# Kernel optimization log

Hardware: AMD Instinct MI355X
Metric: run time of the kernel (lower is better)

## Reference

```python
import jax, jax.numpy as jnp
import numpy as np

N_ACTOR = 128
NUM_MODS = 6
NUM_PTS = 30
N = 32768
B = 64
EPS = 1e-5


def _gn(x, g, b):
    # torch GroupNorm(1, C) on [..., C]: normalize over channel axis, affine
    m = jnp.mean(x, axis=-1, keepdims=True)
    v = jnp.mean((x - m) ** 2, axis=-1, keepdims=True)
    return (x - m) * jax.lax.rsqrt(v + EPS) * g + b


def setup_inputs() -> dict:
    key = jax.random.key(0)
    ks = jax.random.split(key, 32)
    d = N_ACTOR
    M = NUM_MODS
    s = 0.05
    rn = lambda k, shp: jax.random.normal(k, shp, jnp.float32) * s
    inp = {
        'actors': jax.random.normal(ks[0], (N, d), jnp.float32),
        'actor_ctrs': jax.random.normal(ks[1], (N, 2), jnp.float32),
        'actor_idcs': jnp.arange(N, dtype=jnp.int32).reshape(B, N // B),
        # per-mode residual MLP + output linear (stacked over modes)
        'pred_W1': rn(ks[2], (M, d, d)),
        'pred_g1': jnp.ones((M, d), jnp.float32),
        'pred_b1': jnp.zeros((M, d), jnp.float32),
        'pred_W2': rn(ks[3], (M, d, d)),
        'pred_g2': jnp.ones((M, d), jnp.float32),
        'pred_b2': jnp.zeros((M, d), jnp.float32),
        'pred_Wo': rn(ks[4], (M, d, 2 * NUM_PTS)),
        'pred_bo': rn(ks[5], (M, 2 * NUM_PTS)),
        # cls head: residual MLP + Linear(d,1)
        'cls_W1': rn(ks[6], (d, d)),
        'cls_g1': jnp.ones((d,), jnp.float32),
        'cls_b1': jnp.zeros((d,), jnp.float32),
        'cls_W2': rn(ks[7], (d, d)),
        'cls_g2': jnp.ones((d,), jnp.float32),
        'cls_b2': jnp.zeros((d,), jnp.float32),
        'cls_Wo': rn(ks[8], (d, 1)),
        'cls_bo': rn(ks[9], (1,)),
        # AttDest
        'att_dW1': rn(ks[10], (2, d)),
        'att_db1': rn(ks[11], (d,)),
        'att_dW2': rn(ks[12], (d, d)),
        'att_dg2': jnp.ones((d,), jnp.float32),
        'att_db2': jnp.zeros((d,), jnp.float32),
        'att_aW': rn(ks[13], (2 * d, d)),
        'att_ag': jnp.ones((d,), jnp.float32),
        'att_ab': jnp.zeros((d,), jnp.float32),
    }
    return inp


def reference(actors, actor_ctrs, actor_idcs, pred_W1, pred_g1, pred_b1,
              pred_W2, pred_g2, pred_b2, pred_Wo, pred_bo,
              cls_W1, cls_g1, cls_b1, cls_W2, cls_g2, cls_b2, cls_Wo, cls_bo,
              att_dW1, att_db1, att_dW2, att_dg2, att_db2,
              att_aW, att_ag, att_ab):
    n = actors.shape[0]
    M = pred_W1.shape[0]
    h = jnp.einsum('nc,mcd->mnd', actors, pred_W1)              # [M,N,d]
    h = jax.nn.relu(_gn(h, pred_g1[:, None, :], pred_b1[:, None, :]))
    h = _gn(jnp.einsum('mnd,mde->mne', h, pred_W2),
            pred_g2[:, None, :], pred_b2[:, None, :])
    h = jax.nn.relu(h + actors[None])                           # residual
    preds = jnp.einsum('mnd,mdo->mno', h, pred_Wo) + pred_bo[:, None, :]
    reg = preds.transpose(1, 0, 2).reshape(n, M, NUM_PTS, 2)    # [N,M,T,2]
    # per-scene reg[idcs] += ctrs: actor_idcs partitions arange(N), so this
    # is exactly a per-actor broadcast add of the (concatenated) centers
    reg = reg + actor_ctrs[:, None, None, :]
    dest_ctrs = jax.lax.stop_gradient(reg[:, :, -1, :])         # .detach()
    # --- AttDest ---
    dist = (actor_ctrs[:, None, :] - dest_ctrs).reshape(-1, 2)  # [N*M,2]
    dist = jax.nn.relu(dist @ att_dW1 + att_db1)
    dist = jax.nn.relu(_gn(dist @ att_dW2, att_dg2, att_db2))
    agts = jnp.broadcast_to(actors[:, None, :], (n, M, actors.shape[1]))
    agts = agts.reshape(-1, actors.shape[1])
    feats = jax.nn.relu(_gn(jnp.concatenate([dist, agts], axis=1) @ att_aW,
                            att_ag, att_ab))                    # [N*M,d]
    # --- cls head ---
    c = jax.nn.relu(_gn(feats @ cls_W1, cls_g1, cls_b1))
    c = _gn(c @ cls_W2, cls_g2, cls_b2)
    c = jax.nn.relu(c + feats)
    cls = (c @ cls_Wo + cls_bo).reshape(n, M)
    # --- sort modes by descending score, reorder reg accordingly ---
    order = jnp.argsort(-cls, axis=1)
    cls = jnp.take_along_axis(cls, order, axis=1)
    reg = jnp.take_along_axis(reg, order[:, :, None, None], axis=1)
    # train_model=True concatenates the per-scene splits back in order,
    # which reproduces the full arrays
    return cls, reg
```

## Files before the change

kernel.cpp:

```cpp
#include <hip/hip_runtime.h>

#define EPSV 1e-5f
#define CLS_SZ (32768*6)

#define AIDX(k,r) (((k)<<6) + ((r) ^ (((k)&15)<<2)))

__device__ __forceinline__ float4 ld4(const float* p) { return *reinterpret_cast<const float4*>(p); }
__device__ __forceinline__ void st4(float* p, float4 v) { *reinterpret_cast<float4*>(p) = v; }

__device__ __forceinline__ void fma48(float4 x, float4 wl, float4 wh, float acc[4][8]) {
  float av[4] = {x.x, x.y, x.z, x.w};
  float wv[8] = {wl.x, wl.y, wl.z, wl.w, wh.x, wh.y, wh.z, wh.w};
  #pragma unroll
  for (int r = 0; r < 4; ++r)
    #pragma unroll
    for (int c = 0; c < 8; ++c)
      acc[r][c] = fmaf(av[r], wv[c], acc[r][c]);
}

__device__ __forceinline__ void gemm128c(const float* __restrict__ X,
                                         const float* __restrict__ Wg,
                                         float* __restrict__ WB0, float* __restrict__ WB1,
                                         float acc[4][8], int ag4, int jg4, int tid)
{
  float4 rA = ld4(Wg + tid*4);
  float4 rB = ld4(Wg + 1024 + tid*4);
  __syncthreads();
  st4(WB0 + tid*4, rA);
  st4(WB1 + tid*4, rB);
  __syncthreads();
  #pragma unroll 1
  for (int c = 0; c < 16; ++c) {
    float4 rN;
    const bool pf = (c + 2 < 16);
    if (pf) rN = ld4(Wg + (c+2)*1024 + tid*4);
    const float* WB = (c & 1) ? WB1 : WB0;
    #pragma unroll
    for (int kk = 0; kk < 8; ++kk) {
      int k = c*8 + kk;
      float4 x  = ld4(X + ((k<<6) + (ag4 ^ ((k&15)<<2))));
      float4 wl = ld4(WB + (kk<<7) + jg4);
      float4 wh = ld4(WB + (kk<<7) + 64 + jg4);
      fma48(x, wl, wh, acc);
    }
    __syncthreads();
    if (pf) st4(((c & 1) ? WB1 : WB0) + tid*4, rN);
  }
}

__device__ __forceinline__ void gemm128wo(const float* __restrict__ X,
                                          const float* __restrict__ Wg,
                                          float* __restrict__ WB0, float* __restrict__ WB1,
                                          float acc[4][4], int ag4, int jg4, int tid)
{
  const bool act = tid < 120;
  const int row = tid / 15, col = (tid % 15) * 4;
  float4 rA, rB;
  if (act) { rA = ld4(Wg + row*60 + col); rB = ld4(Wg + 480 + row*60 + col); }
  __syncthreads();
  if (act) { st4(WB0 + (row<<6) + col, rA); st4(WB1 + (row<<6) + col, rB); }
  __syncthreads();
  #pragma unroll 1
  for (int c = 0; c < 16; ++c) {
    float4 rN;
    const bool pf = act && (c + 2 < 16);
    if (pf) rN = ld4(Wg + (c+2)*480 + row*60 + col);
    const float* WB = (c & 1) ? WB1 : WB0;
    #pragma unroll
    for (int kk = 0; kk < 8; ++kk) {
      int k = c*8 + kk;
      float4 x = ld4(X + ((k<<6) + (ag4 ^ ((k&15)<<2))));
      float4 w = ld4(WB + (kk<<6) + jg4);
      float av[4] = {x.x, x.y, x.z, x.w};
      float wv[4] = {w.x, w.y, w.z, w.w};
      #pragma unroll
      for (int r = 0; r < 4; ++r)
        #pragma unroll
        for (int cc = 0; cc < 4; ++cc)
          acc[r][cc] = fmaf(av[r], wv[cc], acc[r][cc]);
    }
    __syncthreads();
    if (pf) st4(((c & 1) ? WB1 : WB0) + (row<<6) + col, rN);
  }
}

__device__ __forceinline__ void gn_reduce(const float acc[4][8], float* PS1, float* PS2,
                                          float* MEAN, float* RSTD, int ag4, int jg, int tid)
{
  #pragma unroll
  for (int r = 0; r < 4; ++r) {
    float s = 0.f, q = 0.f;
    #pragma unroll
    for (int c = 0; c < 8; ++c) { float v = acc[r][c]; s += v; q += v*v; }
    s += __shfl_xor(s, 1, 64); q += __shfl_xor(q, 1, 64);
    s += __shfl_xor(s, 2, 64); q += __shfl_xor(q, 2, 64);
    PS1[(ag4+r)*5 + (jg>>2)] = s;
    PS2[(ag4+r)*5 + (jg>>2)] = q;
  }
  __syncthreads();
  if (tid < 64) {
    float a = 0.f, b = 0.f;
    #pragma unroll
    for (int j = 0; j < 4; ++j) { a += PS1[tid*5 + j]; b += PS2[tid*5 + j]; }
    float mu = a * 0.0078125f;
    float var = b * 0.0078125f - mu*mu;
    MEAN[tid] = mu;
    RSTD[tid] = rsqrtf(var + EPSV);
  }
  __syncthreads();
}

__global__ void __launch_bounds__(256) pred_kernel(
    const float* __restrict__ actors, const float* __restrict__ ctrs,
    const float* __restrict__ W1, const float* __restrict__ g1v, const float* __restrict__ b1v,
    const float* __restrict__ W2, const float* __restrict__ g2v, const float* __restrict__ b2v,
    const float* __restrict__ Wo, const float* __restrict__ bov,
    float* __restrict__ out_reg)
{
  __shared__ __align__(16) float ACTORS[8192];
  __shared__ __align__(16) float ACT[8192];
  __shared__ __align__(16) float WB0[1024], WB1[1024];
  __shared__ float PS1[320], PS2[320], MEAN[64], RSTD[64];

  const int tid = threadIdx.x;
  const int jg = tid & 15, ag = tid >> 4;
  const int jg4 = jg*4, ag4 = ag*4;
  const int m  = blockIdx.y;
  const int n0 = blockIdx.x * 64;

  #pragma unroll
  for (int p = 0; p < 8; ++p) {
    int i = (p<<8) + tid;
    int r = i >> 5, c4 = (i & 31) << 2;
    float4 v = ld4(actors + (size_t)(n0 + r)*128 + c4);
    ACTORS[((c4+0)<<6) + (r ^ ((((c4+0))&15)<<2))] = v.x;
    ACTORS[((c4+1)<<6) + (r ^ ((((c4+1))&15)<<2))] = v.y;
    ACTORS[((c4+2)<<6) + (r ^ ((((c4+2))&15)<<2))] = v.z;
    ACTORS[((c4+3)<<6) + (r ^ ((((c4+3))&15)<<2))] = v.w;
  }

  float acc[4][8];
  #pragma unroll
  for (int r = 0; r < 4; ++r)
    #pragma unroll
    for (int c = 0; c < 8; ++c) acc[r][c] = 0.f;

  gemm128c(ACTORS, W1 + (size_t)m*16384, WB0, WB1, acc, ag4, jg4, tid);
  gn_reduce(acc, PS1, PS2, MEAN, RSTD, ag4, jg, tid);
  {
    float mu[4], rs[4];
    #pragma unroll
    for (int r = 0; r < 4; ++r) { mu[r] = MEAN[ag4+r]; rs[r] = RSTD[ag4+r]; }
    #pragma unroll
    for (int c = 0; c < 8; ++c) {
      int ch = (c < 4) ? (jg4 + c) : (64 + jg4 + (c - 4));
      float g = g1v[m*128 + ch], b = b1v[m*128 + ch];
      float4 v;
      v.x = fmaxf((acc[0][c] - mu[0]) * rs[0] * g + b, 0.f);
      v.y = fmaxf((acc[1][c] - mu[1]) * rs[1] * g + b, 0.f);
      v.z = fmaxf((acc[2][c] - mu[2]) * rs[2] * g + b, 0.f);
      v.w = fmaxf((acc[3][c] - mu[3]) * rs[3] * g + b, 0.f);
      st4(ACT + (ch<<6) + (ag4 ^ ((ch&15)<<2)), v);
    }
  }

  #pragma unroll
  for (int r = 0; r < 4; ++r)
    #pragma unroll
    for (int c = 0; c < 8; ++c) acc[r][c] = 0.f;

  gemm128c(ACT, W2 + (size_t)m*16384, WB0, WB1, acc, ag4, jg4, tid);
  gn_reduce(acc, PS1, PS2, MEAN, RSTD, ag4, jg, tid);
  {
    float mu[4], rs[4];
    #pragma unroll
    for (int r = 0; r < 4; ++r) { mu[r] = MEAN[ag4+r]; rs[r] = RSTD[ag4+r]; }
    #pragma unroll
    for (int c = 0; c < 8; ++c) {
      int ch = (c < 4) ? (jg4 + c) : (64 + jg4 + (c - 4));
      float g = g2v[m*128 + ch], b = b2v[m*128 + ch];
      float4 a = ld4(ACTORS + (ch<<6) + (ag4 ^ ((ch&15)<<2)));
      float4 v;
      v.x = fmaxf((acc[0][c] - mu[0]) * rs[0] * g + b + a.x, 0.f);
      v.y = fmaxf((acc[1][c] - mu[1]) * rs[1] * g + b + a.y, 0.f);
      v.z = fmaxf((acc[2][c] - mu[2]) * rs[2] * g + b + a.z, 0.f);
      v.w = fmaxf((acc[3][c] - mu[3]) * rs[3] * g + b + a.w, 0.f);
      st4(ACT + (ch<<6) + (ag4 ^ ((ch&15)<<2)), v);
    }
  }

  float acc2[4][4];
  #pragma unroll
  for (int r = 0; r < 4; ++r)
    #pragma unroll
    for (int c = 0; c < 4; ++c) acc2[r][c] = 0.f;
  gemm128wo(ACT, Wo + (size_t)m*7680, WB0, WB1, acc2, ag4, jg4, tid);

  if (jg < 15) {
    float4 bo4 = ld4(bov + m*60 + jg4);
    #pragma unroll
    for (int r = 0; r < 4; ++r) {
      int n = n0 + ag4 + r;
      float2 cc = *reinterpret_cast<const float2*>(ctrs + 2*n);
      float4 v;
      v.x = acc2[r][0] + bo4.x + cc.x;
      v.y = acc2[r][1] + bo4.y + cc.y;
      v.z = acc2[r][2] + bo4.z + cc.x;
      v.w = acc2[r][3] + bo4.w + cc.y;
      st4(out_reg + (size_t)n*360 + m*60 + jg4, v);
    }
  }
}

__global__ void __launch_bounds__(256) att_cls_kernel(
    const float* __restrict__ actors, const float* __restrict__ ctrs,
    const float* __restrict__ dW1, const float* __restrict__ db1,
    const float* __restrict__ dW2, const float* __restrict__ dg2, const float* __restrict__ db2,
    const float* __restrict__ aW, const float* __restrict__ aG, const float* __restrict__ aB,
    const float* __restrict__ cW1, const float* __restrict__ cg1, const float* __restrict__ cb1,
    const float* __restrict__ cW2, const float* __restrict__ cg2, const float* __restrict__ cb2,
    const float* __restrict__ cWo, const float* __restrict__ cbo,
    const float* __restrict__ reg, float* __restrict__ cls_out)
{
  __shared__ __align__(16) float ACT[8192];
  __shared__ __align__(16) float FEATS[8192];
  __shared__ __align__(16) float WB0[1024], WB1[1024];
  __shared__ float PS1[320], PS2[320], MEAN[64], RSTD[64], D0x[64], D0y[64];

  const int tid = threadIdx.x;
  const int jg = tid & 15, ag = tid >> 4;
  const int jg4 = jg*4, ag4 = ag*4;
  const int r0 = blockIdx.x * 64;

  if (tid < 64) {
    int rg = r0 + tid;
    int n = rg / 6, mm = rg - 6*n;
    size_t base = (size_t)n*360 + mm*60;
    float2 c2 = *reinterpret_cast<const float2*>(ctrs + 2*n);
    D0x[tid] = c2.x - reg[base + 58];
    D0y[tid] = c2.y - reg[base + 59];
  }
  #pragma unroll
  for (int p = 0; p < 8; ++p) {
    int i = (p<<8) + tid;
    int r = i >> 5, c4 = (i & 31) << 2;
    int n = (r0 + r) / 6;
    float4 v = ld4(actors + (size_t)n*128 + c4);
    FEATS[((c4+0)<<6) + (r ^ ((((c4+0))&15)<<2))] = v.x;
    FEATS[((c4+1)<<6) + (r ^ ((((c4+1))&15)<<2))] = v.y;
    FEATS[((c4+2)<<6) + (r ^ ((((c4+2))&15)<<2))] = v.z;
    FEATS[((c4+3)<<6) + (r ^ ((((c4+3))&15)<<2))] = v.w;
  }
  __syncthreads();

  {
    float dx[4], dy[4];
    #pragma unroll
    for (int r = 0; r < 4; ++r) { dx[r] = D0x[ag4+r]; dy[r] = D0y[ag4+r]; }
    #pragma unroll
    for (int c = 0; c < 8; ++c) {
      int ch = (c < 4) ? (jg4 + c) : (64 + jg4 + (c - 4));
      float w1 = dW1[ch], w2 = dW1[128 + ch], bb = db1[ch];
      float4 v;
      v.x = fmaxf(fmaf(dx[0], w1, fmaf(dy[0], w2, bb)), 0.f);
      v.y = fmaxf(fmaf(dx[1], w1, fmaf(dy[1], w2, bb)), 0.f);
      v.z = fmaxf(fmaf(dx[2], w1, fmaf(dy[2], w2, bb)), 0.f);
      v.w = fmaxf(fmaf(dx[3], w1, fmaf(dy[3], w2, bb)), 0.f);
      st4(ACT + (ch<<6) + (ag4 ^ ((ch&15)<<2)), v);
    }
  }

  float acc[4][8];
  #pragma unroll
  for (int r = 0; r < 4; ++r)
    #pragma unroll
    for (int c = 0; c < 8; ++c) acc[r][c] = 0.f;

  gemm128c(ACT, dW2, WB0, WB1, acc, ag4, jg4, tid);
  gn_reduce(acc, PS1, PS2, MEAN, RSTD, ag4, jg, tid);
  {
    float mu[4], rs[4];
    #pragma unroll
    for (int r = 0; r < 4; ++r) { mu[r] = MEAN[ag4+r]; rs[r] = RSTD[ag4+r]; }
    #pragma unroll
    for (int c = 0; c < 8; ++c) {
      int ch = (c < 4) ? (jg4 + c) : (64 + jg4 + (c - 4));
      float g = dg2[ch], b = db2[ch];
      float4 v;
      v.x = fmaxf((acc[0][c] - mu[0]) * rs[0] * g + b, 0.f);
      v.y = fmaxf((acc[1][c] - mu[1]) * rs[1] * g + b, 0.f);
      v.z = fmaxf((acc[2][c] - mu[2]) * rs[2] * g + b, 0.f);
      v.w = fmaxf((acc[3][c] - mu[3]) * rs[3] * g + b, 0.f);
      st4(ACT + (ch<<6) + (ag4 ^ ((ch&15)<<2)), v);
    }
  }

  #pragma unroll
  for (int r = 0; r < 4; ++r)
    #pragma unroll
    for (int c = 0; c < 8; ++c) acc[r][c] = 0.f;
  gemm128c(ACT,   aW,            WB0, WB1, acc, ag4, jg4, tid);
  gemm128c(FEATS, aW + 128*128,  WB0, WB1, acc, ag4, jg4, tid);
  gn_reduce(acc, PS1, PS2, MEAN, RSTD, ag4, jg, tid);
  {
    float mu[4], rs[4];
    #pragma unroll
    for (int r = 0; r < 4; ++r) { mu[r] = MEAN[ag4+r]; rs[r] = RSTD[ag4+r]; }
    #pragma unroll
    for (int c = 0; c < 8; ++c) {
      int ch = (c < 4) ? (jg4 + c) : (64 + jg4 + (c - 4));
      float g = aG[ch], b = aB[ch];
      float4 v;
      v.x = fmaxf((acc[0][c] - mu[0]) * rs[0] * g + b, 0.f);
      v.y = fmaxf((acc[1][c] - mu[1]) * rs[1] * g + b, 0.f);
      v.z = fmaxf((acc[2][c] - mu[2]) * rs[2] * g + b, 0.f);
      v.w = fmaxf((acc[3][c] - mu[3]) * rs[3] * g + b, 0.f);
      st4(ACT   + (ch<<6) + (ag4 ^ ((ch&15)<<2)), v);
      st4(FEATS + (ch<<6) + (ag4 ^ ((ch&15)<<2)), v);
    }
  }

  #pragma unroll
  for (int r = 0; r < 4; ++r)
    #pragma unroll
    for (int c = 0; c < 8; ++c) acc[r][c] = 0.f;
  gemm128c(ACT, cW1, WB0, WB1, acc, ag4, jg4, tid);
  gn_reduce(acc, PS1, PS2, MEAN, RSTD, ag4, jg, tid);
  {
    float mu[4], rs[4];
    #pragma unroll
    for (int r = 0; r < 4; ++r) { mu[r] = MEAN[ag4+r]; rs[r] = RSTD[ag4+r]; }
    #pragma unroll
    for (int c = 0; c < 8; ++c) {
      int ch = (c < 4) ? (jg4 + c) : (64 + jg4 + (c - 4));
      float g = cg1[ch], b = cb1[ch];
      float4 v;
      v.x = fmaxf((acc[0][c] - mu[0]) * rs[0] * g + b, 0.f);
      v.y = fmaxf((acc[1][c] - mu[1]) * rs[1] * g + b, 0.f);
      v.z = fmaxf((acc[2][c] - mu[2]) * rs[2] * g + b, 0.f);
      v.w = fmaxf((acc[3][c] - mu[3]) * rs[3] * g + b, 0.f);
      st4(ACT + (ch<<6) + (ag4 ^ ((ch&15)<<2)), v);
    }
  }

  #pragma unroll
  for (int r = 0; r < 4; ++r)
    #pragma unroll
    for (int c = 0; c < 8; ++c) acc[r][c] = 0.f;
  gemm128c(ACT, cW2, WB0, WB1, acc, ag4, jg4, tid);
  gn_reduce(acc, PS1, PS2, MEAN, RSTD, ag4, jg, tid);
  {
    float mu[4], rs[4], p[4] = {0.f, 0.f, 0.f, 0.f};
    #pragma unroll
    for (int r = 0; r < 4; ++r) { mu[r] = MEAN[ag4+r]; rs[r] = RSTD[ag4+r]; }
    #pragma unroll
    for (int c = 0; c < 8; ++c) {
      int ch = (c < 4) ? (jg4 + c) : (64 + jg4 + (c - 4));
      float g = cg2[ch], b = cb2[ch], wo = cWo[ch];
      float4 f = ld4(FEATS + (ch<<6) + (ag4 ^ ((ch&15)<<2)));
      p[0] = fmaf(fmaxf((acc[0][c] - mu[0]) * rs[0] * g + b + f.x, 0.f), wo, p[0]);
      p[1] = fmaf(fmaxf((acc[1][c] - mu[1]) * rs[1] * g + b + f.y, 0.f), wo, p[1]);
      p[2] = fmaf(fmaxf((acc[2][c] - mu[2]) * rs[2] * g + b + f.z, 0.f), wo, p[2]);
      p[3] = fmaf(fmaxf((acc[3][c] - mu[3]) * rs[3] * g + b + f.w, 0.f), wo, p[3]);
    }
    #pragma unroll
    for (int r = 0; r < 4; ++r) {
      float s = p[r];
      s += __shfl_xor(s, 1, 64);
      s += __shfl_xor(s, 2, 64);
      PS1[(ag4+r)*5 + (jg>>2)] = s;
    }
  }
  __syncthreads();
  if (tid < 64) {
    float s = 0.f;
    #pragma unroll
    for (int j = 0; j < 4; ++j) s += PS1[tid*5 + j];
    cls_out[r0 + tid] = s + cbo[0];
  }
}

__global__ void __launch_bounds__(256) sort_kernel(float* __restrict__ out)
{
  __shared__ float RL[64*360];
  __shared__ float CL[64*6];
  __shared__ float CS[64*6];
  __shared__ int   ORD[64*6];

  const int tid = threadIdx.x;
  const int n0 = blockIdx.x * 64;
  float* regp = out + CLS_SZ;

  for (int i = tid; i < 64*360; i += 256) RL[i] = regp[(size_t)n0*360 + i];
  for (int i = tid; i < 384; i += 256)    CL[i] = out[n0*6 + i];
  __syncthreads();

  if (tid < 64) {
    float v[6];
    #pragma unroll
    for (int m2 = 0; m2 < 6; ++m2) v[m2] = CL[tid*6 + m2];
    int used = 0;
    for (int j = 0; j < 6; ++j) {
      int best = -1; float bv = 0.f;
      for (int m2 = 0; m2 < 6; ++m2) {
        if (used & (1 << m2)) continue;
        if (best < 0 || v[m2] > bv) { best = m2; bv = v[m2]; }
      }
      used |= (1 << best);
      ORD[tid*6 + j] = best;
      CS[tid*6 + j] = bv;
    }
  }
  __syncthreads();

  for (int i = tid; i < 384; i += 256) out[n0*6 + i] = CS[i];
  for (int i = tid; i < 64*360; i += 256) {
    int rl = i / 360, rem = i - rl*360;
    int slot = rem / 60, j = rem - slot*60;
    out[CLS_SZ + (size_t)n0*360 + i] = RL[rl*360 + ORD[rl*6 + slot]*60 + j];
  }
}

extern "C" void kernel_launch(void* const* d_in, const int* in_sizes, int n_in,
                              void* d_out, int out_size, void* d_ws, size_t ws_size,
                              hipStream_t stream)
{
  (void)in_sizes; (void)n_in; (void)out_size; (void)d_ws; (void)ws_size;
  const float* actors = (const float*)d_in[0];
  const float* ctrs   = (const float*)d_in[1];
  const float* pW1 = (const float*)d_in[3];
  const float* pg1 = (const float*)d_in[4];
  const float* pb1 = (const float*)d_in[5];
  const float* pW2 = (const float*)d_in[6];
  const float* pg2 = (const float*)d_in[7];
  const float* pb2 = (const float*)d_in[8];
  const float* pWo = (const float*)d_in[9];
  const float* pbo = (const float*)d_in[10];
  const float* cW1 = (const float*)d_in[11];
  const float* cg1 = (const float*)d_in[12];
  const float* cb1 = (const float*)d_in[13];
  const float* cW2 = (const float*)d_in[14];
  const float* cg2 = (const float*)d_in[15];
  const float* cb2 = (const float*)d_in[16];
  const float* cWo = (const float*)d_in[17];
  const float* cbo = (const float*)d_in[18];
  const float* dW1 = (const float*)d_in[19];
  const float* db1 = (const float*)d_in[20];
  const float* dW2 = (const float*)d_in[21];
  const float* dg2 = (const float*)d_in[22];
  const float* db2 = (const float*)d_in[23];
  const float* aW  = (const float*)d_in[24];
  const float* aG  = (const float*)d_in[25];
  const float* aB  = (const float*)d_in[26];

  float* out = (float*)d_out;
  float* out_reg = out + CLS_SZ;

  dim3 gA(512, 6);
  pred_kernel<<<gA, 256, 0, stream>>>(actors, ctrs, pW1, pg1, pb1, pW2, pg2, pb2,
                                      pWo, pbo, out_reg);
  att_cls_kernel<<<3072, 256, 0, stream>>>(actors, ctrs,
                                           dW1, db1, dW2, dg2, db2,
                                           aW, aG, aB,
                                           cW1, cg1, cb1, cW2, cg2, cb2, cWo, cbo,
                                           out_reg, out);
  sort_kernel<<<512, 256, 0, stream>>>(out);
}
```

Measured before the change: 768.6 us.

## Double rows per block, use 8x8 register tiles and share one LDS buffer

```diff
diff --git a/kernel.cpp b/kernel.cpp
--- a/kernel.cpp
+++ b/kernel.cpp
@@ -3,25 +3,14 @@
 #define EPSV 1e-5f
 #define CLS_SZ (32768*6)
 
-#define AIDX(k,r) (((k)<<6) + ((r) ^ (((k)&15)<<2)))
+#define AL(ch,row) (((ch)<<7) + ((row) ^ ((((ch)&15))<<3)))
 
 __device__ __forceinline__ float4 ld4(const float* p) { return *reinterpret_cast<const float4*>(p); }
 __device__ __forceinline__ void st4(float* p, float4 v) { *reinterpret_cast<float4*>(p) = v; }
 
-__device__ __forceinline__ void fma48(float4 x, float4 wl, float4 wh, float acc[4][8]) {
-  float av[4] = {x.x, x.y, x.z, x.w};
-  float wv[8] = {wl.x, wl.y, wl.z, wl.w, wh.x, wh.y, wh.z, wh.w};
-  #pragma unroll
-  for (int r = 0; r < 4; ++r)
-    #pragma unroll
-    for (int c = 0; c < 8; ++c)
-      acc[r][c] = fmaf(av[r], wv[c], acc[r][c]);
-}
-
-__device__ __forceinline__ void gemm128c(const float* __restrict__ X,
-                                         const float* __restrict__ Wg,
-                                         float* __restrict__ WB0, float* __restrict__ WB1,
-                                         float acc[4][8], int ag4, int jg4, int tid)
+__device__ __forceinline__ void gemmA(const float* X, const float* __restrict__ Wg,
+                                      float* WB0, float* WB1, float (&acc)[8][8],
+                                      int ag, int jg4, int tid)
 {
   float4 rA = ld4(Wg + tid*4);
   float4 rB = ld4(Wg + 1024 + tid*4);
@@ -38,67 +27,100 @@
     #pragma unroll
     for (int kk = 0; kk < 8; ++kk) {
       int k = c*8 + kk;
-      float4 x  = ld4(X + ((k<<6) + (ag4 ^ ((k&15)<<2))));
+      const float* xp = X + (k<<7) + ((ag<<3) ^ ((k & 15)<<3));
+      float4 x0 = ld4(xp), x1 = ld4(xp + 4);
       float4 wl = ld4(WB + (kk<<7) + jg4);
       float4 wh = ld4(WB + (kk<<7) + 64 + jg4);
-      fma48(x, wl, wh, acc);
+      float xv[8] = {x0.x,x0.y,x0.z,x0.w,x1.x,x1.y,x1.z,x1.w};
+      float wv[8] = {wl.x,wl.y,wl.z,wl.w,wh.x,wh.y,wh.z,wh.w};
+      #pragma unroll
+      for (int r = 0; r < 8; ++r)
+        #pragma unroll
+        for (int c2 = 0; c2 < 8; ++c2)
+          acc[r][c2] = fmaf(xv[r], wv[c2], acc[r][c2]);
     }
     __syncthreads();
     if (pf) st4(((c & 1) ? WB1 : WB0) + tid*4, rN);
   }
 }
 
-__device__ __forceinline__ void gemm128wo(const float* __restrict__ X,
-                                          const float* __restrict__ Wg,
-                                          float* __restrict__ WB0, float* __restrict__ WB1,
-                                          float acc[4][4], int ag4, int jg4, int tid)
-{
-  const bool act = tid < 120;
-  const int row = tid / 15, col = (tid % 15) * 4;
+__device__ __forceinline__ void gemmB(const float* X, const float* __restrict__ Wg,
+                                      float* WB0, float* WB1, float (&acc)[4][8],
+                                      int ag, int jg4, int tid)
+{
   float4 rA, rB;
-  if (act) { rA = ld4(Wg + row*60 + col); rB = ld4(Wg + 480 + row*60 + col); }
-  __syncthreads();
-  if (act) { st4(WB0 + (row<<6) + col, rA); st4(WB1 + (row<<6) + col, rB); }
+  const bool wload = tid < 256;
+  if (wload) { rA = ld4(Wg + tid*4); rB = ld4(Wg + 1024 + tid*4); }
+  __syncthreads();
+  if (wload) { st4(WB0 + tid*4, rA); st4(WB1 + tid*4, rB); }
   __syncthreads();
   #pragma unroll 1
   for (int c = 0; c < 16; ++c) {
     float4 rN;
-    const bool pf = act && (c + 2 < 16);
-    if (pf) rN = ld4(Wg + (c+2)*480 + row*60 + col);
+    const bool pf = wload && (c + 2 < 16);
+    if (pf) rN = ld4(Wg + (c+2)*1024 + tid*4);
     const float* WB = (c & 1) ? WB1 : WB0;
     #pragma unroll
     for (int kk = 0; kk < 8; ++kk) {
       int k = c*8 + kk;
-      float4 x = ld4(X + ((k<<6) + (ag4 ^ ((k&15)<<2))));
-      float4 w = ld4(WB + (kk<<6) + jg4);
-      float av[4] = {x.x, x.y, x.z, x.w};
-      float wv[4] = {w.x, w.y, w.z, w.w};
+      float4 x = ld4(X + (k<<7) + ((ag<<2) ^ ((k & 15)<<3)));
+      float4 wl = ld4(WB + (kk<<7) + jg4);
+      float4 wh = ld4(WB + (kk<<7) + 64 + jg4);
+      float xv[4] = {x.x,x.y,x.z,x.w};
+      float wv[8] = {wl.x,wl.y,wl.z,wl.w,wh.x,wh.y,wh.z,wh.w};
       #pragma unroll
       for (int r = 0; r < 4; ++r)
         #pragma unroll
-        for (int cc = 0; cc < 4; ++cc)
-          acc[r][cc] = fmaf(av[r], wv[cc], acc[r][cc]);
+        for (int c2 = 0; c2 < 8; ++c2)
+          acc[r][c2] = fmaf(xv[r], wv[c2], acc[r][c2]);
     }
     __syncthreads();
-    if (pf) st4(((c & 1) ? WB1 : WB0) + (row<<6) + col, rN);
-  }
-}
-
-__device__ __forceinline__ void gn_reduce(const float acc[4][8], float* PS1, float* PS2,
-                                          float* MEAN, float* RSTD, int ag4, int jg, int tid)
-{
-  #pragma unroll
-  for (int r = 0; r < 4; ++r) {
-    float s = 0.f, q = 0.f;
-    #pragma unroll
-    for (int c = 0; c < 8; ++c) { float v = acc[r][c]; s += v; q += v*v; }
-    s += __shfl_xor(s, 1, 64); q += __shfl_xor(q, 1, 64);
-    s += __shfl_xor(s, 2, 64); q += __shfl_xor(q, 2, 64);
-    PS1[(ag4+r)*5 + (jg>>2)] = s;
-    PS2[(ag4+r)*5 + (jg>>2)] = q;
-  }
-  __syncthreads();
-  if (tid < 64) {
+    if (pf) st4(((c & 1) ? WB1 : WB0) + tid*4, rN);
+  }
+}
+
+__device__ __forceinline__ void gemmWo(const float* X, const float* __restrict__ Wg,
+                                       float* WB0, float* WB1, float (&acc)[8][4],
+                                       int ag, int jg, int tid)
+{
+  const bool ld = tid < 120;
+  const bool zp = (tid >= 120 && tid < 128);
+  const int kk0 = ld ? (tid / 15) : (tid - 120);
+  const int sl  = ld ? (tid % 15) * 4 : 60;
+  float4 rA = {0,0,0,0}, rB = {0,0,0,0};
+  if (ld) { rA = ld4(Wg + kk0*60 + sl); rB = ld4(Wg + 480 + kk0*60 + sl); }
+  __syncthreads();
+  if (ld || zp) { st4(WB0 + (kk0<<6) + sl, rA); st4(WB1 + (kk0<<6) + sl, rB); }
+  __syncthreads();
+  #pragma unroll 1
+  for (int c = 0; c < 16; ++c) {
+    float4 rN = {0,0,0,0};
+    const bool pf = (c + 2 < 16);
+    if (pf && ld) rN = ld4(Wg + (c+2)*480 + kk0*60 + sl);
+    const float* WB = (c & 1) ? WB1 : WB0;
+    #pragma unroll
+    for (int kk = 0; kk < 8; ++kk) {
+      int k = c*8 + kk;
+      const float* xp = X + (k<<7) + ((ag<<3) ^ ((k & 15)<<3));
+      float4 x0 = ld4(xp), x1 = ld4(xp + 4);
+      float4 w = ld4(WB + (kk<<6) + jg*4);
+      float xv[8] = {x0.x,x0.y,x0.z,x0.w,x1.x,x1.y,x1.z,x1.w};
+      float wv[4] = {w.x,w.y,w.z,w.w};
+      #pragma unroll
+      for (int r = 0; r < 8; ++r)
+        #pragma unroll
+        for (int c2 = 0; c2 < 4; ++c2)
+          acc[r][c2] = fmaf(xv[r], wv[c2], acc[r][c2]);
+    }
+    __syncthreads();
+    if (pf && (ld || zp)) st4(((c & 1) ? WB1 : WB0) + (kk0<<6) + sl, rN);
+  }
+}
+
+__device__ __forceinline__ void gn_finish(float* PS1, float* PS2, float* MEAN, float* RSTD, int tid)
+{
+  __syncthreads();
+  if (tid < 128) {
     float a = 0.f, b = 0.f;
     #pragma unroll
     for (int j = 0; j < 4; ++j) { a += PS1[tid*5 + j]; b += PS2[tid*5 + j]; }
@@ -110,97 +132,139 @@
   __syncthreads();
 }
 
-__global__ void __launch_bounds__(256) pred_kernel(
+__device__ __forceinline__ void gn_reduce8(const float (&acc)[8][8], float* PS1, float* PS2,
+                                           float* MEAN, float* RSTD, int ag, int jg, int tid)
+{
+  #pragma unroll
+  for (int r = 0; r < 8; ++r) {
+    float s = 0.f, q = 0.f;
+    #pragma unroll
+    for (int c = 0; c < 8; ++c) { float v = acc[r][c]; s += v; q += v*v; }
+    s += __shfl_xor(s, 1, 64); q += __shfl_xor(q, 1, 64);
+    s += __shfl_xor(s, 2, 64); q += __shfl_xor(q, 2, 64);
+    if ((jg & 3) == 0) { int row = ag*8 + r; PS1[row*5 + (jg>>2)] = s; PS2[row*5 + (jg>>2)] = q; }
+  }
+  gn_finish(PS1, PS2, MEAN, RSTD, tid);
+}
+
+__device__ __forceinline__ void gn_reduce4(const float (&acc)[4][8], float* PS1, float* PS2,
+                                           float* MEAN, float* RSTD, int ag, int jg, int tid)
+{
+  #pragma unroll
+  for (int r = 0; r < 4; ++r) {
+    float s = 0.f, q = 0.f;
+    #pragma unroll
+    for (int c = 0; c < 8; ++c) { float v = acc[r][c]; s += v; q += v*v; }
+    s += __shfl_xor(s, 1, 64); q += __shfl_xor(q, 1, 64);
+    s += __shfl_xor(s, 2, 64); q += __shfl_xor(q, 2, 64);
+    if ((jg & 3) == 0) { int row = ag*4 + r; PS1[row*5 + (jg>>2)] = s; PS2[row*5 + (jg>>2)] = q; }
+  }
+  gn_finish(PS1, PS2, MEAN, RSTD, tid);
+}
+
+__global__ void __launch_bounds__(256, 2) pred_kernel(
     const float* __restrict__ actors, const float* __restrict__ ctrs,
     const float* __restrict__ W1, const float* __restrict__ g1v, const float* __restrict__ b1v,
     const float* __restrict__ W2, const float* __restrict__ g2v, const float* __restrict__ b2v,
     const float* __restrict__ Wo, const float* __restrict__ bov,
     float* __restrict__ out_reg)
 {
-  __shared__ __align__(16) float ACTORS[8192];
-  __shared__ __align__(16) float ACT[8192];
+  __shared__ __align__(16) float ACT[16384];
   __shared__ __align__(16) float WB0[1024], WB1[1024];
-  __shared__ float PS1[320], PS2[320], MEAN[64], RSTD[64];
+  __shared__ float PS1[640], PS2[640], MEAN[128], RSTD[128];
 
   const int tid = threadIdx.x;
   const int jg = tid & 15, ag = tid >> 4;
-  const int jg4 = jg*4, ag4 = ag*4;
+  const int jg4 = jg*4;
   const int m  = blockIdx.y;
-  const int n0 = blockIdx.x * 64;
-
-  #pragma unroll
-  for (int p = 0; p < 8; ++p) {
+  const int n0 = blockIdx.x * 128;
+
+  #pragma unroll
+  for (int p = 0; p < 16; ++p) {
     int i = (p<<8) + tid;
-    int r = i >> 5, c4 = (i & 31) << 2;
-    float4 v = ld4(actors + (size_t)(n0 + r)*128 + c4);
-    ACTORS[((c4+0)<<6) + (r ^ ((((c4+0))&15)<<2))] = v.x;
-    ACTORS[((c4+1)<<6) + (r ^ ((((c4+1))&15)<<2))] = v.y;
-    ACTORS[((c4+2)<<6) + (r ^ ((((c4+2))&15)<<2))] = v.z;
-    ACTORS[((c4+3)<<6) + (r ^ ((((c4+3))&15)<<2))] = v.w;
-  }
-
-  float acc[4][8];
-  #pragma unroll
-  for (int r = 0; r < 4; ++r)
+    int r = i >> 5, q4 = (i & 31) << 2;
+    float4 v = ld4(actors + (size_t)(n0 + r)*128 + q4);
+    ACT[AL(q4+0, r)] = v.x; ACT[AL(q4+1, r)] = v.y;
+    ACT[AL(q4+2, r)] = v.z; ACT[AL(q4+3, r)] = v.w;
+  }
+
+  float acc[8][8];
+  #pragma unroll
+  for (int r = 0; r < 8; ++r)
     #pragma unroll
     for (int c = 0; c < 8; ++c) acc[r][c] = 0.f;
 
-  gemm128c(ACTORS, W1 + (size_t)m*16384, WB0, WB1, acc, ag4, jg4, tid);
-  gn_reduce(acc, PS1, PS2, MEAN, RSTD, ag4, jg, tid);
-  {
-    float mu[4], rs[4];
-    #pragma unroll
-    for (int r = 0; r < 4; ++r) { mu[r] = MEAN[ag4+r]; rs[r] = RSTD[ag4+r]; }
+  gemmA(ACT, W1 + (size_t)m*16384, WB0, WB1, acc, ag, jg4, tid);
+  gn_reduce8(acc, PS1, PS2, MEAN, RSTD, ag, jg, tid);
+  {
+    float mu[8], rs[8];
+    #pragma unroll
+    for (int r = 0; r < 8; ++r) { mu[r] = MEAN[ag*8+r]; rs[r] = RSTD[ag*8+r]; }
+    float4 gl = ld4(g1v + m*128 + jg4), gh = ld4(g1v + m*128 + 64 + jg4);
+    float4 bl = ld4(b1v + m*128 + jg4), bh = ld4(b1v + m*128 + 64 + jg4);
+    float gv[8] = {gl.x,gl.y,gl.z,gl.w,gh.x,gh.y,gh.z,gh.w};
+    float bv[8] = {bl.x,bl.y,bl.z,bl.w,bh.x,bh.y,bh.z,bh.w};
+    float vm[8][8];
+    #pragma unroll
+    for (int r = 0; r < 8; ++r)
+      #pragma unroll
+      for (int c = 0; c < 8; ++c)
+        vm[r][c] = fmaxf((acc[r][c] - mu[r]) * rs[r] * gv[c] + bv[c], 0.f);
     #pragma unroll
     for (int c = 0; c < 8; ++c) {
       int ch = (c < 4) ? (jg4 + c) : (64 + jg4 + (c - 4));
-      float g = g1v[m*128 + ch], b = b1v[m*128 + ch];
-      float4 v;
-      v.x = fmaxf((acc[0][c] - mu[0]) * rs[0] * g + b, 0.f);
-      v.y = fmaxf((acc[1][c] - mu[1]) * rs[1] * g + b, 0.f);
-      v.z = fmaxf((acc[2][c] - mu[2]) * rs[2] * g + b, 0.f);
-      v.w = fmaxf((acc[3][c] - mu[3]) * rs[3] * g + b, 0.f);
-      st4(ACT + (ch<<6) + (ag4 ^ ((ch&15)<<2)), v);
-    }
-  }
-
-  #pragma unroll
-  for (int r = 0; r < 4; ++r)
+      int base = (ch<<7) + ((ag<<3) ^ ((ch & 15)<<3));
+      st4(ACT + base,     make_float4(vm[0][c],vm[1][c],vm[2][c],vm[3][c]));
+      st4(ACT + base + 4, make_float4(vm[4][c],vm[5][c],vm[6][c],vm[7][c]));
+    }
+  }
+
+  #pragma unroll
+  for (int r = 0; r < 8; ++r)
     #pragma unroll
     for (int c = 0; c < 8; ++c) acc[r][c] = 0.f;
 
-  gemm128c(ACT, W2 + (size_t)m*16384, WB0, WB1, acc, ag4, jg4, tid);
-  gn_reduce(acc, PS1, PS2, MEAN, RSTD, ag4, jg, tid);
-  {
-    float mu[4], rs[4];
-    #pragma unroll
-    for (int r = 0; r < 4; ++r) { mu[r] = MEAN[ag4+r]; rs[r] = RSTD[ag4+r]; }
+  gemmA(ACT, W2 + (size_t)m*16384, WB0, WB1, acc, ag, jg4, tid);
+  gn_reduce8(acc, PS1, PS2, MEAN, RSTD, ag, jg, tid);
+  {
+    float mu[8], rs[8];
+    #pragma unroll
+    for (int r = 0; r < 8; ++r) { mu[r] = MEAN[ag*8+r]; rs[r] = RSTD[ag*8+r]; }
+    float4 gl = ld4(g2v + m*128 + jg4), gh = ld4(g2v + m*128 + 64 + jg4);
+    float4 bl = ld4(b2v + m*128 + jg4), bh = ld4(b2v + m*128 + 64 + jg4);
+    float gv[8] = {gl.x,gl.y,gl.z,gl.w,gh.x,gh.y,gh.z,gh.w};
+    float bv[8] = {bl.x,bl.y,bl.z,bl.w,bh.x,bh.y,bh.z,bh.w};
+    float vm[8][8];
+    #pragma unroll
+    for (int r = 0; r < 8; ++r) {
+      const float* ap = actors + (size_t)(n0 + ag*8 + r)*128;
+      float4 a0 = ld4(ap + jg4), a1 = ld4(ap + 64 + jg4);
+      float av[8] = {a0.x,a0.y,a0.z,a0.w,a1.x,a1.y,a1.z,a1.w};
+      #pragma unroll
+      for (int c = 0; c < 8; ++c)
+        vm[r][c] = fmaxf((acc[r][c] - mu[r]) * rs[r] * gv[c] + bv[c] + av[c], 0.f);
+    }
     #pragma unroll
     for (int c = 0; c < 8; ++c) {
       int ch = (c < 4) ? (jg4 + c) : (64 + jg4 + (c - 4));
-      float g = g2v[m*128 + ch], b = b2v[m*128 + ch];
-      float4 a = ld4(ACTORS + (ch<<6) + (ag4 ^ ((ch&15)<<2)));
-      float4 v;
-      v.x = fmaxf((acc[0][c] - mu[0]) * rs[0] * g + b + a.x, 0.f);
-      v.y = fmaxf((acc[1][c] - mu[1]) * rs[1] * g + b + a.y, 0.f);
-      v.z = fmaxf((acc[2][c] - mu[2]) * rs[2] * g + b + a.z, 0.f);
-      v.w = fmaxf((acc[3][c] - mu[3]) * rs[3] * g + b + a.w, 0.f);
-      st4(ACT + (ch<<6) + (ag4 ^ ((ch&15)<<2)), v);
-    }
-  }
-
-  float acc2[4][4];
-  #pragma unroll
-  for (int r = 0; r < 4; ++r)
+      int base = (ch<<7) + ((ag<<3) ^ ((ch & 15)<<3));
+      st4(ACT + base,     make_float4(vm[0][c],vm[1][c],vm[2][c],vm[3][c]));
+      st4(ACT + base + 4, make_float4(vm[4][c],vm[5][c],vm[6][c],vm[7][c]));
+    }
+  }
+
+  float acc2[8][4];
+  #pragma unroll
+  for (int r = 0; r < 8; ++r)
     #pragma unroll
     for (int c = 0; c < 4; ++c) acc2[r][c] = 0.f;
-  gemm128wo(ACT, Wo + (size_t)m*7680, WB0, WB1, acc2, ag4, jg4, tid);
+  gemmWo(ACT, Wo + (size_t)m*7680, WB0, WB1, acc2, ag, jg, tid);
 
   if (jg < 15) {
     float4 bo4 = ld4(bov + m*60 + jg4);
     #pragma unroll
-    for (int r = 0; r < 4; ++r) {
-      int n = n0 + ag4 + r;
+    for (int r = 0; r < 8; ++r) {
+      int n = n0 + ag*8 + r;
       float2 cc = *reinterpret_cast<const float2*>(ctrs + 2*n);
       float4 v;
       v.x = acc2[r][0] + bo4.x + cc.x;
@@ -212,7 +276,7 @@
   }
 }
 
-__global__ void __launch_bounds__(256) att_cls_kernel(
+__global__ void __launch_bounds__(512, 4) att_cls_kernel(
     const float* __restrict__ actors, const float* __restrict__ ctrs,
     const float* __restrict__ dW1, const float* __restrict__ db1,
     const float* __restrict__ dW2, const float* __restrict__ dg2, const float* __restrict__ db2,
@@ -222,17 +286,16 @@
     const float* __restrict__ cWo, const float* __restrict__ cbo,
     const float* __restrict__ reg, float* __restrict__ cls_out)
 {
-  __shared__ __align__(16) float ACT[8192];
-  __shared__ __align__(16) float FEATS[8192];
+  __shared__ __align__(16) float ACT[16384];
   __shared__ __align__(16) float WB0[1024], WB1[1024];
-  __shared__ float PS1[320], PS2[320], MEAN[64], RSTD[64], D0x[64], D0y[64];
+  __shared__ float PS1[640], PS2[640], MEAN[128], RSTD[128], D0x[128], D0y[128];
 
   const int tid = threadIdx.x;
   const int jg = tid & 15, ag = tid >> 4;
-  const int jg4 = jg*4, ag4 = ag*4;
-  const int r0 = blockIdx.x * 64;
-
-  if (tid < 64) {
+  const int jg4 = jg*4;
+  const int r0 = blockIdx.x * 128;
+
+  if (tid < 128) {
     int rg = r0 + tid;
     int n = rg / 6, mm = rg - 6*n;
     size_t base = (size_t)n*360 + mm*60;
@@ -240,23 +303,12 @@
     D0x[tid] = c2.x - reg[base + 58];
     D0y[tid] = c2.y - reg[base + 59];
   }
-  #pragma unroll
-  for (int p = 0; p < 8; ++p) {
-    int i = (p<<8) + tid;
-    int r = i >> 5, c4 = (i & 31) << 2;
-    int n = (r0 + r) / 6;
-    float4 v = ld4(actors + (size_t)n*128 + c4);
-    FEATS[((c4+0)<<6) + (r ^ ((((c4+0))&15)<<2))] = v.x;
-    FEATS[((c4+1)<<6) + (r ^ ((((c4+1))&15)<<2))] = v.y;
-    FEATS[((c4+2)<<6) + (r ^ ((((c4+2))&15)<<2))] = v.z;
-    FEATS[((c4+3)<<6) + (r ^ ((((c4+3))&15)<<2))] = v.w;
-  }
   __syncthreads();
 
   {
     float dx[4], dy[4];
     #pragma unroll
-    for (int r = 0; r < 4; ++r) { dx[r] = D0x[ag4+r]; dy[r] = D0y[ag4+r]; }
+    for (int r = 0; r < 4; ++r) { dx[r] = D0x[ag*4+r]; dy[r] = D0y[ag*4+r]; }
     #pragma unroll
     for (int c = 0; c < 8; ++c) {
       int ch = (c < 4) ? (jg4 + c) : (64 + jg4 + (c - 4));
@@ -266,7 +318,7 @@
       v.y = fmaxf(fmaf(dx[1], w1, fmaf(dy[1], w2, bb)), 0.f);
       v.z = fmaxf(fmaf(dx[2], w1, fmaf(dy[2], w2, bb)), 0.f);
       v.w = fmaxf(fmaf(dx[3], w1, fmaf(dy[3], w2, bb)), 0.f);
-      st4(ACT + (ch<<6) + (ag4 ^ ((ch&15)<<2)), v);
+      st4(ACT + (ch<<7) + ((ag<<2) ^ ((ch & 15)<<3)), v);
     }
   }
 
@@ -276,22 +328,25 @@
     #pragma unroll
     for (int c = 0; c < 8; ++c) acc[r][c] = 0.f;
 
-  gemm128c(ACT, dW2, WB0, WB1, acc, ag4, jg4, tid);
-  gn_reduce(acc, PS1, PS2, MEAN, RSTD, ag4, jg, tid);
+  gemmB(ACT, dW2, WB0, WB1, acc, ag, jg4, tid);
+  gn_reduce4(acc, PS1, PS2, MEAN, RSTD, ag, jg, tid);
   {
     float mu[4], rs[4];
     #pragma unroll
-    for (int r = 0; r < 4; ++r) { mu[r] = MEAN[ag4+r]; rs[r] = RSTD[ag4+r]; }
+    for (int r = 0; r < 4; ++r) { mu[r] = MEAN[ag*4+r]; rs[r] = RSTD[ag*4+r]; }
+    float4 gl = ld4(dg2 + jg4), gh = ld4(dg2 + 64 + jg4);
+    float4 bl = ld4(db2 + jg4), bh = ld4(db2 + 64 + jg4);
+    float gv[8] = {gl.x,gl.y,gl.z,gl.w,gh.x,gh.y,gh.z,gh.w};
+    float bv[8] = {bl.x,bl.y,bl.z,bl.w,bh.x,bh.y,bh.z,bh.w};
     #pragma unroll
     for (int c = 0; c < 8; ++c) {
       int ch = (c < 4) ? (jg4 + c) : (64 + jg4 + (c - 4));
-      float g = dg2[ch], b = db2[ch];
       float4 v;
-      v.x = fmaxf((acc[0][c] - mu[0]) * rs[0] * g + b, 0.f);
-      v.y = fmaxf((acc[1][c] - mu[1]) * rs[1] * g + b, 0.f);
-      v.z = fmaxf((acc[2][c] - mu[2]) * rs[2] * g + b, 0.f);
-      v.w = fmaxf((acc[3][c] - mu[3]) * rs[3] * g + b, 0.f);
-      st4(ACT + (ch<<6) + (ag4 ^ ((ch&15)<<2)), v);
+      v.x = fmaxf((acc[0][c] - mu[0]) * rs[0] * gv[c] + bv[c], 0.f);
+      v.y = fmaxf((acc[1][c] - mu[1]) * rs[1] * gv[c] + bv[c], 0.f);
+      v.z = fmaxf((acc[2][c] - mu[2]) * rs[2] * gv[c] + bv[c], 0.f);
+      v.w = fmaxf((acc[3][c] - mu[3]) * rs[3] * gv[c] + bv[c], 0.f);
+      st4(ACT + (ch<<7) + ((ag<<2) ^ ((ch & 15)<<3)), v);
     }
   }
 
@@ -299,24 +354,63 @@
   for (int r = 0; r < 4; ++r)
     #pragma unroll
     for (int c = 0; c < 8; ++c) acc[r][c] = 0.f;
-  gemm128c(ACT,   aW,            WB0, WB1, acc, ag4, jg4, tid);
-  gemm128c(FEATS, aW + 128*128,  WB0, WB1, acc, ag4, jg4, tid);
-  gn_reduce(acc, PS1, PS2, MEAN, RSTD, ag4, jg, tid);
+  gemmB(ACT, aW, WB0, WB1, acc, ag, jg4, tid);
+  #pragma unroll
+  for (int p = 0; p < 8; ++p) {
+    int i = (p<<9) + tid;
+    int r = i >> 5, q4 = (i & 31) << 2;
+    int n = (r0 + r) / 6;
+    float4 v = ld4(actors + (size_t)n*128 + q4);
+    ACT[AL(q4+0, r)] = v.x; ACT[AL(q4+1, r)] = v.y;
+    ACT[AL(q4+2, r)] = v.z; ACT[AL(q4+3, r)] = v.w;
+  }
+  gemmB(ACT, aW + 16384, WB0, WB1, acc, ag, jg4, tid);
+  gn_reduce4(acc, PS1, PS2, MEAN, RSTD, ag, jg, tid);
+  float feats[4][8];
   {
     float mu[4], rs[4];
     #pragma unroll
-    for (int r = 0; r < 4; ++r) { mu[r] = MEAN[ag4+r]; rs[r] = RSTD[ag4+r]; }
+    for (int r = 0; r < 4; ++r) { mu[r] = MEAN[ag*4+r]; rs[r] = RSTD[ag*4+r]; }
+    float4 gl = ld4(aG + jg4), gh = ld4(aG + 64 + jg4);
+    float4 bl = ld4(aB + jg4), bh = ld4(aB + 64 + jg4);
+    float gv[8] = {gl.x,gl.y,gl.z,gl.w,gh.x,gh.y,gh.z,gh.w};
+    float bv[8] = {bl.x,bl.y,bl.z,bl.w,bh.x,bh.y,bh.z,bh.w};
+    #pragma unroll
+    for (int r = 0; r < 4; ++r)
+      #pragma unroll
+      for (int c = 0; c < 8; ++c)
+        feats[r][c] = fmaxf((acc[r][c] - mu[r]) * rs[r] * gv[c] + bv[c], 0.f);
     #pragma unroll
     for (int c = 0; c < 8; ++c) {
       int ch = (c < 4) ? (jg4 + c) : (64 + jg4 + (c - 4));
-      float g = aG[ch], b = aB[ch];
+      st4(ACT + (ch<<7) + ((ag<<2) ^ ((ch & 15)<<3)),
+          make_float4(feats[0][c],feats[1][c],feats[2][c],feats[3][c]));
+    }
+  }
+
+  #pragma unroll
+  for (int r = 0; r < 4; ++r)
+    #pragma unroll
+    for (int c = 0; c < 8; ++c) acc[r][c] = 0.f;
+  gemmB(ACT, cW1, WB0, WB1, acc, ag, jg4, tid);
+  gn_reduce4(acc, PS1, PS2, MEAN, RSTD, ag, jg, tid);
+  {
+    float mu[4], rs[4];
+    #pragma unroll
+    for (int r = 0; r < 4; ++r) { mu[r] = MEAN[ag*4+r]; rs[r] = RSTD[ag*4+r]; }
+    float4 gl = ld4(cg1 + jg4), gh = ld4(cg1 + 64 + jg4);
+    float4 bl = ld4(cb1 + jg4), bh = ld4(cb1 + 64 + jg4);
+    float gv[8] = {gl.x,gl.y,gl.z,gl.w,gh.x,gh.y,gh.z,gh.w};
+    float bv[8] = {bl.x,bl.y,bl.z,bl.w,bh.x,bh.y,bh.z,bh.w};
+    #pragma unroll
+    for (int c = 0; c < 8; ++c) {
+      int ch = (c < 4) ? (jg4 + c) : (64 + jg4 + (c - 4));
       float4 v;
-      v.x = fmaxf((acc[0][c] - mu[0]) * rs[0] * g + b, 0.f);
-      v.y = fmaxf((acc[1][c] - mu[1]) * rs[1] * g + b, 0.f);
-      v.z = fmaxf((acc[2][c] - mu[2]) * rs[2] * g + b, 0.f);
-      v.w = fmaxf((acc[3][c] - mu[3]) * rs[3] * g + b, 0.f);
-      st4(ACT   + (ch<<6) + (ag4 ^ ((ch&15)<<2)), v);
-      st4(FEATS + (ch<<6) + (ag4 ^ ((ch&15)<<2)), v);
+      v.x = fmaxf((acc[0][c] - mu[0]) * rs[0] * gv[c] + bv[c], 0.f);
+      v.y = fmaxf((acc[1][c] - mu[1]) * rs[1] * gv[c] + bv[c], 0.f);
+      v.z = fmaxf((acc[2][c] - mu[2]) * rs[2] * gv[c] + bv[c], 0.f);
+      v.w = fmaxf((acc[3][c] - mu[3]) * rs[3] * gv[c] + bv[c], 0.f);
+      st4(ACT + (ch<<7) + ((ag<<2) ^ ((ch & 15)<<3)), v);
     }
   }
 
@@ -324,55 +418,35 @@
   for (int r = 0; r < 4; ++r)
     #pragma unroll
     for (int c = 0; c < 8; ++c) acc[r][c] = 0.f;
-  gemm128c(ACT, cW1, WB0, WB1, acc, ag4, jg4, tid);
-  gn_reduce(acc, PS1, PS2, MEAN, RSTD, ag4, jg, tid);
-  {
-    float mu[4], rs[4];
-    #pragma unroll
-    for (int r = 0; r < 4; ++r) { mu[r] = MEAN[ag4+r]; rs[r] = RSTD[ag4+r]; }
-    #pragma unroll
-    for (int c = 0; c < 8; ++c) {
-      int ch = (c < 4) ? (jg4 + c) : (64 + jg4 + (c - 4));
-      float g = cg1[ch], b = cb1[ch];
-      float4 v;
-      v.x = fmaxf((acc[0][c] - mu[0]) * rs[0] * g + b, 0.f);
-      v.y = fmaxf((acc[1][c] - mu[1]) * rs[1] * g + b, 0.f);
-      v.z = fmaxf((acc[2][c] - mu[2]) * rs[2] * g + b, 0.f);
-      v.w = fmaxf((acc[3][c] - mu[3]) * rs[3] * g + b, 0.f);
-      st4(ACT + (ch<<6) + (ag4 ^ ((ch&15)<<2)), v);
-    }
-  }
-
-  #pragma unroll
-  for (int r = 0; r < 4; ++r)
-    #pragma unroll
-    for (int c = 0; c < 8; ++c) acc[r][c] = 0.f;
-  gemm128c(ACT, cW2, WB0, WB1, acc, ag4, jg4, tid);
-  gn_reduce(acc, PS1, PS2, MEAN, RSTD, ag4, jg, tid);
+  gemmB(ACT, cW2, WB0, WB1, acc, ag, jg4, tid);
+  gn_reduce4(acc, PS1, PS2, MEAN, RSTD, ag, jg, tid);
   {
     float mu[4], rs[4], p[4] = {0.f, 0.f, 0.f, 0.f};
     #pragma unroll
-    for (int r = 0; r < 4; ++r) { mu[r] = MEAN[ag4+r]; rs[r] = RSTD[ag4+r]; }
-    #pragma unroll
-    for (int c = 0; c < 8; ++c) {
-      int ch = (c < 4) ? (jg4 + c) : (64 + jg4 + (c - 4));
-      float g = cg2[ch], b = cb2[ch], wo = cWo[ch];
-      float4 f = ld4(FEATS + (ch<<6) + (ag4 ^ ((ch&15)<<2)));
-      p[0] = fmaf(fmaxf((acc[0][c] - mu[0]) * rs[0] * g + b + f.x, 0.f), wo, p[0]);
-      p[1] = fmaf(fmaxf((acc[1][c] - mu[1]) * rs[1] * g + b + f.y, 0.f), wo, p[1]);
-      p[2] = fmaf(fmaxf((acc[2][c] - mu[2]) * rs[2] * g + b + f.z, 0.f), wo, p[2]);
-      p[3] = fmaf(fmaxf((acc[3][c] - mu[3]) * rs[3] * g + b + f.w, 0.f), wo, p[3]);
+    for (int r = 0; r < 4; ++r) { mu[r] = MEAN[ag*4+r]; rs[r] = RSTD[ag*4+r]; }
+    float4 gl = ld4(cg2 + jg4), gh = ld4(cg2 + 64 + jg4);
+    float4 bl = ld4(cb2 + jg4), bh = ld4(cb2 + 64 + jg4);
+    float4 wl = ld4(cWo + jg4), wh = ld4(cWo + 64 + jg4);
+    float gv[8] = {gl.x,gl.y,gl.z,gl.w,gh.x,gh.y,gh.z,gh.w};
+    float bv[8] = {bl.x,bl.y,bl.z,bl.w,bh.x,bh.y,bh.z,bh.w};
+    float wv[8] = {wl.x,wl.y,wl.z,wl.w,wh.x,wh.y,wh.z,wh.w};
+    #pragma unroll
+    for (int c = 0; c < 8; ++c) {
+      p[0] = fmaf(fmaxf((acc[0][c] - mu[0]) * rs[0] * gv[c] + bv[c] + feats[0][c], 0.f), wv[c], p[0]);
+      p[1] = fmaf(fmaxf((acc[1][c] - mu[1]) * rs[1] * gv[c] + bv[c] + feats[1][c], 0.f), wv[c], p[1]);
+      p[2] = fmaf(fmaxf((acc[2][c] - mu[2]) * rs[2] * gv[c] + bv[c] + feats[2][c], 0.f), wv[c], p[2]);
+      p[3] = fmaf(fmaxf((acc[3][c] - mu[3]) * rs[3] * gv[c] + bv[c] + feats[3][c], 0.f), wv[c], p[3]);
     }
     #pragma unroll
     for (int r = 0; r < 4; ++r) {
       float s = p[r];
       s += __shfl_xor(s, 1, 64);
       s += __shfl_xor(s, 2, 64);
-      PS1[(ag4+r)*5 + (jg>>2)] = s;
-    }
-  }
-  __syncthreads();
-  if (tid < 64) {
+      if ((jg & 3) == 0) PS1[(ag*4+r)*5 + (jg>>2)] = s;
+    }
+  }
+  __syncthreads();
+  if (tid < 128) {
     float s = 0.f;
     #pragma unroll
     for (int j = 0; j < 4; ++j) s += PS1[tid*5 + j];
@@ -456,10 +530,10 @@
   float* out = (float*)d_out;
   float* out_reg = out + CLS_SZ;
 
-  dim3 gA(512, 6);
+  dim3 gA(256, 6);
   pred_kernel<<<gA, 256, 0, stream>>>(actors, ctrs, pW1, pg1, pb1, pW2, pg2, pb2,
                                       pWo, pbo, out_reg);
-  att_cls_kernel<<<3072, 256, 0, stream>>>(actors, ctrs,
+  att_cls_kernel<<<1536, 512, 0, stream>>>(actors, ctrs,
                                            dW1, db1, dW2, dg2, db2,
                                            aW, aG, aB,
                                            cW1, cg1, cb1, cW2, cg2, cb2, cWo, cbo,
```

Result: slower. 1.149 ms (+49.5%).
